# Kernel optimization log

Hardware: AMD Instinct MI355X
Metric: run time of the kernel (lower is better)

## Reference

```python
import jax, jax.numpy as jnp
import numpy as np

D_MODEL = 1024
B, T_Q, T_KV = 4, 2048, 2048


def _linear_params(key, d_in, d_out):
    kw, kb = jax.random.split(key)
    W = jax.random.normal(kw, (d_out, d_in), dtype=jnp.float32) * 0.02
    b = jax.random.normal(kb, (d_out,), dtype=jnp.float32) * 0.02
    return W, b


def setup_inputs() -> dict:
    key = jax.random.key(0)
    ks = jax.random.split(key, 7)
    latent_space = jax.random.normal(ks[0], (B, T_Q, D_MODEL), dtype=jnp.float32)
    input_space = jax.random.normal(ks[1], (B, T_KV, D_MODEL), dtype=jnp.float32)
    Wl, bl = _linear_params(ks[2], D_MODEL, D_MODEL)
    Wu, bu = _linear_params(ks[3], D_MODEL, D_MODEL)
    WA, bA = _linear_params(ks[4], D_MODEL, D_MODEL)  # A_proj: d -> J (J = d)
    WV, bV = _linear_params(ks[5], D_MODEL, D_MODEL)  # V_proj: J -> d
    Wo, bo = _linear_params(ks[6], D_MODEL, D_MODEL)
    return {
        "latent_space": latent_space, "input_space": input_space,
        "Wl": Wl, "bl": bl, "Wu": Wu, "bu": bu,
        "WA": WA, "bA": bA, "WV": WV, "bV": bV,
        "Wo": Wo, "bo": bo,
    }


def reference(latent_space, input_space, Wl, bl, Wu, bu, WA, bA, WV, bV, Wo, bo):
    # emb_0 = l_proj(latent)            [B, T_q, d]
    emb0 = jnp.einsum('bqd,ed->bqe', latent_space, Wl) + bl
    # l = softmax(u_proj(emb_0), -1)^T  [B, d, T_q]
    l = jax.nn.softmax(jnp.einsum('bqd,ed->bqe', emb0, Wu) + bu, axis=-1)
    l = jnp.swapaxes(l, -2, -1)
    # D = A_proj(input)                 [B, T_kv, J]
    Dm = jnp.einsum('bkd,jd->bkj', input_space, WA) + bA
    # A = softmax(V_proj(D), dim=-2)    softmax over T_kv
    A = jax.nn.softmax(jnp.einsum('bkj,dj->bkd', Dm, WV) + bV, axis=-2)
    # w = A @ l                         [B, T_kv, T_q]
    w = jnp.einsum('bkd,bdq->bkq', A, l)
    # o = w @ o_proj(latent)            [B, T_kv, d]
    ov = jnp.einsum('bqd,ed->bqe', latent_space, Wo) + bo
    o = jnp.einsum('bkq,bqd->bkd', w, ov)
    return o
```

## Files before the change

### kernel.cpp

```cpp
#include <hip/hip_runtime.h>
#include <hip/hip_bf16.h>
#include <stdint.h>

typedef __attribute__((ext_vector_type(8))) short bf16x8;
typedef __attribute__((ext_vector_type(4))) float f32x4;
typedef __attribute__((ext_vector_type(4))) unsigned short u16x4;

#define B_  4
#define T_  2048
#define D_  1024

__device__ __forceinline__ float bf2f(ushort u) {
  union { unsigned int i; float f; } v; v.i = ((unsigned int)u) << 16; return v.f;
}
__device__ __forceinline__ ushort f2bf(float f) {
  return (ushort)(__bfloat16_as_ushort(__float2bfloat16(f)));
}
__device__ __forceinline__ void async16(const void* g, void* l) {
  __builtin_amdgcn_global_load_lds(
      (const __attribute__((address_space(1))) void*)g,
      (__attribute__((address_space(3))) void*)l, 16, 0, 0);
}

__global__ __launch_bounds__(256)
void prep(const float* __restrict__ lat, const float* __restrict__ inp,
          const float* __restrict__ Wl, const float* __restrict__ bl,
          const float* __restrict__ Wu, const float* __restrict__ bu,
          const float* __restrict__ WA, const float* __restrict__ bA,
          const float* __restrict__ WV, const float* __restrict__ bV,
          const float* __restrict__ Wo, const float* __restrict__ bo,
          ushort* __restrict__ xBf, ushort* __restrict__ xBf2,
          ushort* __restrict__ w1, ushort* __restrict__ w2,
          ushort* __restrict__ wCatWo, float* __restrict__ bc, float* __restrict__ bc2,
          float* __restrict__ psum)
{
  __shared__ alignas(16) ushort t[64 * 65];
  const long NW = (long)D_ * D_;
  const int bx = blockIdx.x;
  const int tid = threadIdx.x;
  if (bx < 16384) {
    const float* in = bx < 8192 ? lat : inp;
    ushort* out = bx < 8192 ? xBf : xBf2;
    const long i = (long)(bx & 8191) * 256 + tid;
    const float4 v = *(const float4*)(in + i * 4);
    u16x4 o;
    o[0] = f2bf(v.x); o[1] = f2bf(v.y); o[2] = f2bf(v.z); o[3] = f2bf(v.w);
    *(u16x4*)(out + i * 4) = o;
  } else if (bx < 19456) {
    const int seg = (bx - 16384) >> 10;
    const float* in  = seg == 0 ? Wu : (seg == 1 ? WV : Wo);
    ushort* out = seg == 0 ? w1 : (seg == 1 ? w1 + NW : wCatWo);
    const long i = (long)((bx - 16384) & 1023) * 256 + tid;
    const float4 v = *(const float4*)(in + i * 4);
    u16x4 o;
    o[0] = f2bf(v.x); o[1] = f2bf(v.y); o[2] = f2bf(v.z); o[3] = f2bf(v.w);
    *(u16x4*)(out + i * 4) = o;
  } else if (bx < 19968) {
    const int z = (bx - 19456) >> 8;
    const int w = (bx - 19456) & 255;
    const float* in = z ? WA : Wl;
    ushort* out = z ? w2 + NW : w2;
    const int c0 = (w & 15) * 64, r0 = (w >> 4) * 64;
    const int tx = tid & 15, ty = tid >> 4;
#pragma unroll
    for (int i = 0; i < 4; ++i) {
      const int r = ty + i * 16;
      const float4 v = *(const float4*)(in + (long)(r0 + r) * D_ + c0 + tx * 4);
      t[(tx * 4 + 0) * 65 + r] = f2bf(v.x);
      t[(tx * 4 + 1) * 65 + r] = f2bf(v.y);
      t[(tx * 4 + 2) * 65 + r] = f2bf(v.z);
      t[(tx * 4 + 3) * 65 + r] = f2bf(v.w);
    }
    __syncthreads();
#pragma unroll
    for (int i = 0; i < 4; ++i) {
      const int c = ty + i * 16;
      u16x4 v;
#pragma unroll
      for (int j = 0; j < 4; ++j) v[j] = t[c * 65 + tx * 4 + j];
      *(u16x4*)(out + (long)(c0 + c) * D_ + r0 + tx * 4) = v;
    }
  } else if (bx < 20480) {
    const int z = (bx - 19968) >> 8;
    const int w = (bx - 19968) & 255;
    const float* W    = z ? WV : Wu;
    const float* bin  = z ? bA : bl;
    const float* badd = z ? bV : bu;
    float* out        = z ? bc2 : bc;
    const int wv = tid >> 6, lane = tid & 63;
    const int e = w * 4 + wv;
    const float* row = W + (long)e * D_;
    float s = 0.f;
#pragma unroll
    for (int i = 0; i < 16; ++i) s += row[lane + i * 64] * bin[lane + i * 64];
#pragma unroll
    for (int off = 32; off; off >>= 1) s += __shfl_xor(s, off);
    if (lane == 0) out[e] = s + badd[e];
  } else {
    psum[(bx - 20480) * 256 + tid] = 0.f;
  }
}

#define PH_SYNC_IN()                                               \
  __builtin_amdgcn_s_barrier();                                    \
  asm volatile("s_waitcnt lgkmcnt(0)" ::: "memory");               \
  __builtin_amdgcn_sched_barrier(0);                               \
  __builtin_amdgcn_s_setprio(1)
#define PH_SYNC_OUT()                                              \
  __builtin_amdgcn_s_setprio(0);                                   \
  __builtin_amdgcn_s_barrier()

__global__ __launch_bounds__(512, 2)
void gemm256(const ushort* __restrict__ A, const ushort* __restrict__ Bm,
             const float* __restrict__ bias1, const float* __restrict__ bias2,
             ushort* __restrict__ C1, ushort* __restrict__ C2,
             int ldA, int ldB)
{
  __shared__ alignas(16) ushort AbS[2 * 16384];
  __shared__ alignas(16) ushort BbS[3 * 16384];

  const int gx = gridDim.x;
  const int nwg = gx * gridDim.y;
  int fid = blockIdx.y * gx + blockIdx.x;
  fid = (fid & 7) * (nwg >> 3) + (fid >> 3);
  const int bx = fid % gx;
  const int by = fid / gx;
  const int tileM = by * 256, tileN = bx * 256;

  const int tid  = threadIdx.x;
  const int wid  = tid >> 6;
  const int lane = tid & 63;
  const int wm   = wid >> 2;
  const int wn   = wid & 3;

  const int srow8 = tid >> 3;
  const int scol8 = ((tid & 7) ^ (srow8 & 7)) << 3;
  const ushort* gAs = A  + (long)(tileM + srow8) * ldA + scol8;
  const ushort* gBs = Bm + (long)(tileN + srow8) * ldB + scol8;
  const int sdst = tid << 3;

#define STA(b, i, t) async16(gAs + (long)((i) * 64) * ldA + (t) * 64, \
                             AbS + (b) * 16384 + (i) * 4096 + sdst)
#define STB(b, i, t) async16(gBs + (long)((i) * 64) * ldB + (t) * 64, \
                             BbS + (b) * 16384 + (i) * 4096 + sdst)

  const int frow = lane & 15;
  const int kg   = lane >> 4;
  const int ck0 = ((kg       ^ (frow & 7)) << 3);
  const int ck1 = (((4 + kg) ^ (frow & 7)) << 3);
  int aoffr[8], boffr[4];
#pragma unroll
  for (int mi = 0; mi < 8; ++mi) aoffr[mi] = (wm * 128 + mi * 16 + frow) * 64;
#pragma unroll
  for (int n = 0; n < 4; ++n)    boffr[n]  = (wn * 64 + n * 16 + frow) * 64;

  f32x4 acc[8][4];
#pragma unroll
  for (int i = 0; i < 8; ++i)
#pragma unroll
    for (int j = 0; j < 4; ++j) acc[i][j] = (f32x4){0.f, 0.f, 0.f, 0.f};

#pragma unroll
  for (int i = 0; i < 4; ++i) STA(0, i, 0);
#pragma unroll
  for (int i = 0; i < 4; ++i) STB(0, i, 0);
#pragma unroll
  for (int i = 0; i < 4; ++i) STA(1, i, 1);
#pragma unroll
  for (int i = 0; i < 4; ++i) STB(1, i, 1);
  asm volatile("s_waitcnt vmcnt(8)" ::: "memory");
  __builtin_amdgcn_s_barrier();

#pragma unroll 1
  for (int t = 0; t < 16; ++t) {
    const int buf = t & 1;
    const int bB  = t - (t / 3) * 3;
    const int nA  = (t + 1) & 1;
    const int nB  = (t + 2) - ((t + 2) / 3) * 3;
    const ushort* Ac = AbS + buf * 16384;
    const ushort* Bc = BbS + bB * 16384;
    bf16x8 fa[4], fb[4], ga[4];

#pragma unroll
    for (int n = 0; n < 4; ++n) fb[n] = *(const bf16x8*)(Bc + boffr[n] + ck0);
#pragma unroll
    for (int m = 0; m < 4; ++m) fa[m] = *(const bf16x8*)(Ac + aoffr[m] + ck0);
    if (t >= 1 && t <= 14) { STA(nA, 0, t + 1); STA(nA, 1, t + 1); }
    PH_SYNC_IN();
#pragma unroll
    for (int m = 0; m < 4; ++m)
#pragma unroll
      for (int n = 0; n < 4; ++n)
        acc[m][n] = __builtin_amdgcn_mfma_f32_16x16x32_bf16(fa[m], fb[n], acc[m][n], 0, 0, 0);
    PH_SYNC_OUT();

#pragma unroll
    for (int m = 0; m < 4; ++m) ga[m] = *(const bf16x8*)(Ac + aoffr[4 + m] + ck0);
    if (t >= 1 && t <= 14) { STA(nA, 2, t + 1); STA(nA, 3, t + 1); }
    if (t <= 13)           { STB(nB, 0, t + 2); STB(nB, 1, t + 2); }
    PH_SYNC_IN();
#pragma unroll
    for (int m = 0; m < 4; ++m)
#pragma unroll
      for (int n = 0; n < 4; ++n)
        acc[4 + m][n] = __builtin_amdgcn_mfma_f32_16x16x32_bf16(ga[m], fb[n], acc[4 + m][n], 0, 0, 0);
    PH_SYNC_OUT();

#pragma unroll
    for (int n = 0; n < 4; ++n) fb[n] = *(const bf16x8*)(Bc + boffr[n] + ck1);
#pragma unroll
    for (int m = 0; m < 4; ++m) fa[m] = *(const bf16x8*)(Ac + aoffr[m] + ck1);
    if (t <= 13) { STB(nB, 2, t + 2); STB(nB, 3, t + 2); }
    PH_SYNC_IN();
#pragma unroll
    for (int m = 0; m < 4; ++m)
#pragma unroll
      for (int n = 0; n < 4; ++n)
        acc[m][n] = __builtin_amdgcn_mfma_f32_16x16x32_bf16(fa[m], fb[n], acc[m][n], 0, 0, 0);
    PH_SYNC_OUT();

#pragma unroll
    for (int m = 0; m < 4; ++m) ga[m] = *(const bf16x8*)(Ac + aoffr[4 + m] + ck1);
    if (t <= 13)      { asm volatile("s_waitcnt vmcnt(4)" ::: "memory"); }
    else if (t == 14) { asm volatile("s_waitcnt vmcnt(0)" ::: "memory"); }
    PH_SYNC_IN();
#pragma unroll
    for (int m = 0; m < 4; ++m)
#pragma unroll
      for (int n = 0; n < 4; ++n)
        acc[4 + m][n] = __builtin_amdgcn_mfma_f32_16x16x32_bf16(ga[m], fb[n], acc[4 + m][n], 0, 0, 0);
    PH_SYNC_OUT();
  }
#undef STA
#undef STB

  const bool second = tileN >= 1024;
  ushort* Cp = second ? C2 : C1;
  const float* bb = second ? bias2 : bias1;
  const int cb = tileN - (second ? 1024 : 0) + wn * 64 + (lane & 15);
  const int rb = tileM + wm * 128 + ((lane >> 4) << 2);
#pragma unroll
  for (int mi = 0; mi < 8; ++mi) {
    const int mrow = rb + mi * 16;
#pragma unroll
    for (int ni = 0; ni < 4; ++ni) {
      const int col = cb + ni * 16;
      const float bv = bb[col];
#pragma unroll
      for (int r = 0; r < 4; ++r)
        Cp[(long)(mrow + r) * 1024 + col] = f2bf(acc[mi][ni][r] + bv);
    }
  }
}

template<int MODE, int NKT = 16>
__global__ __launch_bounds__(512, 2)
void gemm128(const ushort* __restrict__ A, const ushort* __restrict__ Bm,
             const float* __restrict__ bias1, void* __restrict__ C1,
             int ldA, int ldB, long sAz, long sBz, long sCz,
             float* __restrict__ psumG)
{
  __shared__ alignas(16) ushort AbS[3 * 16384];
  __shared__ alignas(16) ushort BbS[3 * 8192];

  const int gx = gridDim.x, gy = gridDim.y;
  const int nwg = gx * gy * gridDim.z;
  int fid = (blockIdx.z * gy + blockIdx.y) * gx + blockIdx.x;
  fid = (fid & 7) * (nwg >> 3) + (fid >> 3);
  const int bx = fid % gx;
  const int by = (fid / gx) % gy;
  const int bz = fid / (gx * gy);
  const int tileM = by * 256, tileN = bx * 128;

  const ushort* Ap = A;
  const ushort* Bp = Bm;
  if constexpr (MODE == 2) {
    Ap += (long)(bz >> 1) * sAz + (long)(bz & 1) * 1024;
    Bp += (long)(bz >> 1) * sBz + (long)(bz & 1) * 1024;
  } else if constexpr (MODE == 4) {
    Ap += (long)(bz >> 2) * sAz + (long)(bz & 3) * 256;
    Bp += (long)(bz >> 2) * sBz + (long)(bz & 3) * 256;
  } else {
    Ap += (long)bz * sAz;
    Bp += (long)bz * sBz;
  }

  const int tid  = threadIdx.x;
  const int wid  = tid >> 6;
  const int lane = tid & 63;
  const int wm   = wid >> 1;
  const int wn   = wid & 1;

  const int srow8 = tid >> 3;
  const int scol8 = ((tid & 7) ^ (srow8 & 7)) << 3;
  const ushort* gAs = Ap + (long)(tileM + srow8) * ldA + scol8;
  const ushort* gBs = Bp + (long)(tileN + srow8) * ldB + scol8;
  const int sdst = tid << 3;

#define STA(b, i, t) async16(gAs + (long)((i) * 64) * ldA + (t) * 64, \
                             AbS + (b) * 16384 + (i) * 4096 + sdst)
#define STB(b, i, t) async16(gBs + (long)((i) * 64) * ldB + (t) * 64, \
                             BbS + (b) * 8192 + (i) * 4096 + sdst)

  const int frow = lane & 15;
  const int kg   = lane >> 4;
  const int ck0 = ((kg       ^ (frow & 7)) << 3);
  const int ck1 = (((4 + kg) ^ (frow & 7)) << 3);
  int aoffr[4], boffr[4];
#pragma unroll
  for (int mi = 0; mi < 4; ++mi) aoffr[mi] = (wm * 64 + mi * 16 + frow) * 64;
#pragma unroll
  for (int n = 0; n < 4; ++n)    boffr[n]  = (wn * 64 + n * 16 + frow) * 64;

  f32x4 acc[4][4];
#pragma unroll
  for (int i = 0; i < 4; ++i)
#pragma unroll
    for (int j = 0; j < 4; ++j) acc[i][j] = (f32x4){0.f, 0.f, 0.f, 0.f};

#pragma unroll
  for (int i = 0; i < 4; ++i) STA(0, i, 0);
  STB(0, 0, 0); STB(0, 1, 0);
#pragma unroll
  for (int i = 0; i < 4; ++i) STA(1, i, 1);
  STB(1, 0, 1); STB(1, 1, 1);
  asm volatile("s_waitcnt vmcnt(6)" ::: "memory");
  __builtin_amdgcn_s_barrier();

#pragma unroll 1
  for (int t = 0; t < NKT; ++t) {
    const int bufT = t - (t / 3) * 3;
    const int nb   = (t + 2) - ((t + 2) / 3) * 3;
    const ushort* Ac = AbS + bufT * 16384;
    const ushort* Bc = BbS + bufT * 8192;
    bf16x8 fa[4], fb[4];

#pragma unroll
    for (int n = 0; n < 4; ++n) fb[n] = *(const bf16x8*)(Bc + boffr[n] + ck0);
#pragma unroll
    for (int m = 0; m < 4; ++m) fa[m] = *(const bf16x8*)(Ac + aoffr[m] + ck0);
    if (t <= NKT - 3) { STA(nb, 0, t + 2); STA(nb, 1, t + 2); STA(nb, 2, t + 2); STA(nb, 3, t + 2); }
    PH_SYNC_IN();
#pragma unroll
    for (int m = 0; m < 4; ++m)
#pragma unroll
      for (int n = 0; n < 4; ++n)
        acc[m][n] = __builtin_amdgcn_mfma_f32_16x16x32_bf16(fa[m], fb[n], acc[m][n], 0, 0, 0);
    PH_SYNC_OUT();

#pragma unroll
    for (int n = 0; n < 4; ++n) fb[n] = *(const bf16x8*)(Bc + boffr[n] + ck1);
#pragma unroll
    for (int m = 0; m < 4; ++m) fa[m] = *(const bf16x8*)(Ac + aoffr[m] + ck1);
    if (t <= NKT - 3) { STB(nb, 0, t + 2); STB(nb, 1, t + 2); }
    if (t <= NKT - 3)      { asm volatile("s_waitcnt vmcnt(6)" ::: "memory"); }
    else if (t == NKT - 2) { asm volatile("s_waitcnt vmcnt(0)" ::: "memory"); }
    PH_SYNC_IN();
#pragma unroll
    for (int m = 0; m < 4; ++m)
#pragma unroll
      for (int n = 0; n < 4; ++n)
        acc[m][n] = __builtin_amdgcn_mfma_f32_16x16x32_bf16(fa[m], fb[n], acc[m][n], 0, 0, 0);
    PH_SYNC_OUT();
  }
#undef STA
#undef STB

  const int cb = tileN + wn * 64 + (lane & 15);
  const int rb = tileM + wm * 64 + ((lane >> 4) << 2);

  if constexpr (MODE == 1) {
    ushort* Cp = (ushort*)C1;
    const int bE = tileM >> 11;
#pragma unroll
    for (int ni = 0; ni < 4; ++ni) {
      const int col = cb + ni * 16;
      const float bv = bias1[col];
      float cs = 0.f;
#pragma unroll
      for (int mi = 0; mi < 4; ++mi)
#pragma unroll
        for (int r = 0; r < 4; ++r) {
          const ushort ev = f2bf(__expf(acc[mi][ni][r] + bv));
          Cp[(long)(rb + mi * 16 + r) * 1024 + col] = ev;
          cs += bf2f(ev);
        }
      cs += __shfl_xor(cs, 16);
      cs += __shfl_xor(cs, 32);
      if ((lane >> 4) == 0) atomicAdd(psumG + (long)bE * D_ + col, cs);
    }
  } else if constexpr (MODE == 2) {
    ushort* Cp = (ushort*)C1 + ((long)(bz & 1) * B_ + (bz >> 1)) * ((long)D_ * D_);
#pragma unroll
    for (int ni = 0; ni < 4; ++ni) {
      const int col = cb + ni * 16;
#pragma unroll
      for (int mi = 0; mi < 4; ++mi)
#pragma unroll
        for (int r = 0; r < 4; ++r)
          Cp[(long)(rb + mi * 16 + r) * 1024 + col] = f2bf(acc[mi][ni][r]);
    }
  } else if constexpr (MODE == 4) {
    const int comp = bz >> 2, sp = bz & 3;
    ushort* Cp = (ushort*)C1 + ((long)sp * 2 + comp) * ((long)D_ * D_);
#pragma unroll
    for (int ni = 0; ni < 4; ++ni) {
      const int col = cb + ni * 16;
#pragma unroll
      for (int mi = 0; mi < 4; ++mi)
#pragma unroll
        for (int r = 0; r < 4; ++r)
          Cp[(long)(rb + mi * 16 + r) * 1024 + col] = f2bf(acc[mi][ni][r]);
    }
  } else {
    float* Cp = (float*)C1 + (long)bz * sCz;
#pragma unroll
    for (int ni = 0; ni < 4; ++ni) {
      const int col = cb + ni * 16;
#pragma unroll
      for (int mi = 0; mi < 4; ++mi)
#pragma unroll
        for (int r = 0; r < 4; ++r)
          Cp[(long)(rb + mi * 16 + r) * 1024 + col] = acc[mi][ni][r];
    }
  }
}

__global__ __launch_bounds__(256)
void reduce4(const ushort* __restrict__ P, ushort* __restrict__ wCat)
{
  const long NW = (long)D_ * D_;
  const long i = ((long)blockIdx.x * 256 + threadIdx.x) * 8;
  float s[8] = {0.f, 0.f, 0.f, 0.f, 0.f, 0.f, 0.f, 0.f};
#pragma unroll
  for (int sp = 0; sp < 4; ++sp) {
    bf16x8 p = *(const bf16x8*)(P + (long)sp * 2 * NW + i);
#pragma unroll
    for (int j = 0; j < 8; ++j) s[j] += bf2f((ushort)p[j]);
  }
  const long comp = (i >= NW) ? 1 : 0;
  ushort* out = wCat + comp * 2 * NW + (i - comp * NW);
  bf16x8 o;
#pragma unroll
  for (int j = 0; j < 8; ++j) o[j] = (short)f2bf(s[j]);
  *(bf16x8*)out = o;
}

__global__ __launch_bounds__(256)
void rowexp_inv(const ushort* __restrict__ S, float* __restrict__ rinv)
{
  const long base = (long)blockIdx.x * D_;
  const int tid = threadIdx.x;
  float s = 0.f;
#pragma unroll
  for (int i = 0; i < 4; ++i) s += __expf(bf2f(S[base + i * 256 + tid]));
#pragma unroll
  for (int off = 32; off; off >>= 1) s += __shfl_xor(s, off);
  __shared__ float reds[4];
  if ((tid & 63) == 0) reds[tid >> 6] = s;
  __syncthreads();
  if (tid == 0) rinv[blockIdx.x] = 1.f / (reds[0] + reds[1] + reds[2] + reds[3]);
}

__global__ __launch_bounds__(256)
void transposeF(const ushort* __restrict__ l, ushort* __restrict__ lT,
                const ushort* __restrict__ ov, ushort* __restrict__ ovT,
                const float* __restrict__ rinv)
{
  __shared__ alignas(16) ushort t[64 * 65];
  const int z = blockIdx.z;
  const int b = z & (B_ - 1);
  const bool isL = z < B_;
  const ushort* in = (isL ? l : ov) + (long)b * T_ * D_;
  ushort* out      = (isL ? lT : ovT) + (long)b * (long)D_ * T_;
  const int c0 = blockIdx.x * 64, r0 = blockIdx.y * 64;
  const int tx = threadIdx.x & 15, ty = threadIdx.x >> 4;
#pragma unroll
  for (int i = 0; i < 4; ++i) {
    const int r = ty + i * 16;
    u16x4 v = *(const u16x4*)(in + (long)(r0 + r) * D_ + c0 + tx * 4);
    if (isL) {
      const float ri = rinv[(long)b * T_ + r0 + r];
#pragma unroll
      for (int c = 0; c < 4; ++c) t[(tx * 4 + c) * 65 + r] = f2bf(__expf(bf2f(v[c])) * ri);
    } else {
#pragma unroll
      for (int c = 0; c < 4; ++c) t[(tx * 4 + c) * 65 + r] = v[c];
    }
  }
  __syncthreads();
#pragma unroll
  for (int i = 0; i < 4; ++i) {
    const int c = ty + i * 16;
    u16x4 v;
#pragma unroll
    for (int j = 0; j < 4; ++j) v[j] = t[c * 65 + tx * 4 + j];
    *(u16x4*)(out + (long)(c0 + c) * T_ + r0 + tx * 4) = v;
  }
}

__global__ __launch_bounds__(256)
void reduce2_scale(const ushort* __restrict__ P, const float* __restrict__ psum,
                   ushort* __restrict__ MT)
{
  const long stride = (long)B_ * D_ * D_;
  const long base = ((long)blockIdx.x * 256 + threadIdx.x) * 8;
  const int b = (int)(base >> 20);
  const int e0 = (int)(base & (D_ - 1));
  bf16x8 p0 = *(const bf16x8*)(P + base);
  bf16x8 p1 = *(const bf16x8*)(P + stride + base);
  const float4 c0 = *(const float4*)(psum + (long)b * D_ + e0);
  const float4 c1 = *(const float4*)(psum + (long)b * D_ + e0 + 4);
  const float cc[8] = {1.f / c0.x, 1.f / c0.y, 1.f / c0.z, 1.f / c0.w,
                       1.f / c1.x, 1.f / c1.y, 1.f / c1.z, 1.f / c1.w};
  bf16x8 o;
#pragma unroll
  for (int j = 0; j < 8; ++j)
    o[j] = (short)f2bf((bf2f((ushort)p0[j]) + bf2f((ushort)p1[j])) * cc[j]);
  *(bf16x8*)(MT + base) = o;
}

extern "C" void kernel_launch(void* const* d_in, const int* in_sizes, int n_in,
                              void* d_out, int out_size, void* d_ws, size_t ws_size,
                              hipStream_t stream)
{
  (void)in_sizes; (void)n_in; (void)out_size; (void)ws_size;
  const float* lat = (const float*)d_in[0];
  const float* inp = (const float*)d_in[1];
  const float* Wl  = (const float*)d_in[2];
  const float* bl  = (const float*)d_in[3];
  const float* Wu  = (const float*)d_in[4];
  const float* bu  = (const float*)d_in[5];
  const float* WA  = (const float*)d_in[6];
  const float* bA  = (const float*)d_in[7];
  const float* WV  = (const float*)d_in[8];
  const float* bV  = (const float*)d_in[9];
  const float* Wo  = (const float*)d_in[10];
  const float* bo  = (const float*)d_in[11];

  char* w = (char*)d_ws;
  auto carve = [&](size_t bytes) { char* p = w; w += (bytes + 255) & ~(size_t)255; return p; };
  const long NT = (long)B_ * T_ * D_;
  const long NW = (long)D_ * D_;
  ushort* xBf   = (ushort*)carve(NT * 2);
  ushort* xBf2  = (ushort*)carve(NT * 2);
  ushort* bufA  = (ushort*)carve(NT * 2);
  ushort* bufB  = (ushort*)carve(NT * 2);
  ushort* scr   = (ushort*)carve(NT * 2);
  ushort* MT    = (ushort*)carve((long)B_ * NW * 2);
  ushort* wCat  = (ushort*)carve(3 * NW * 2);
  float*  bc    = (float*)carve(D_ * 4);
  float*  bc2   = (float*)carve(D_ * 4);
  float*  psum  = (float*)carve((long)B_ * D_ * 4);
  float*  rinv  = (float*)carve((long)B_ * T_ * 4);
  ushort* w1 = scr;
  ushort* w2 = scr + 2 * NW;
  ushort* Pc = bufA;
  ushort* ovT = scr;
  ushort* part = bufB;

  const dim3 blk(256, 1, 1);
  const dim3 blk5(512, 1, 1);

  prep<<<dim3(20496), blk, 0, stream>>>(lat, inp, Wl, bl, Wu, bu, WA, bA, WV, bV, Wo, bo,
                                        xBf, xBf2, w1, w2, wCat + NW, bc, bc2, psum);
  gemm128<4, 4><<<dim3(8, 4, 8), blk5, 0, stream>>>(
      w1, w2, nullptr, Pc, D_, D_, NW, NW, 0, nullptr);
  reduce4<<<dim3(1024), blk, 0, stream>>>(Pc, wCat);
  gemm256<<<dim3(8, 32, 1), blk5, 0, stream>>>(
      xBf, wCat, bc, bo, bufB, bufA, D_, D_);
  rowexp_inv<<<dim3(B_ * T_), blk, 0, stream>>>(bufB, rinv);
  transposeF<<<dim3(16, 32, 2 * B_), blk, 0, stream>>>(bufB, xBf, bufA, ovT, rinv);
  gemm128<2><<<dim3(8, 4, 8), blk5, 0, stream>>>(
      ovT, xBf, nullptr, part, T_, T_, (long)D_ * T_, (long)D_ * T_, 0, nullptr);
  gemm128<1><<<dim3(8, 32, 1), blk5, 0, stream>>>(
      xBf2, wCat + 2 * NW, bc2, bufA, D_, D_, 0, 0, 0, psum);
  reduce2_scale<<<dim3(2048), blk, 0, stream>>>(part, psum, MT);
  gemm128<3><<<dim3(8, 8, 4), blk5, 0, stream>>>(
      bufA, MT, nullptr, d_out, D_, D_,
      (long)T_ * D_, NW, (long)T_ * D_, nullptr);
}
```

Baseline: 292.0 us.

## Fuse row-exp sums into GEMM epilogue and merge two GEMMs into one launch

```diff
diff --git a/kernel.cpp b/kernel.cpp
--- a/kernel.cpp
+++ b/kernel.cpp
@@ -114,7 +114,7 @@
 void gemm256(const ushort* __restrict__ A, const ushort* __restrict__ Bm,
              const float* __restrict__ bias1, const float* __restrict__ bias2,
              ushort* __restrict__ C1, ushort* __restrict__ C2,
-             int ldA, int ldB)
+             int ldA, int ldB, float* __restrict__ rsumP)
 {
   __shared__ alignas(16) ushort AbS[2 * 16384];
   __shared__ alignas(16) ushort BbS[3 * 16384];
@@ -239,16 +239,46 @@
   const float* bb = second ? bias2 : bias1;
   const int cb = tileN - (second ? 1024 : 0) + wn * 64 + (lane & 15);
   const int rb = tileM + wm * 128 + ((lane >> 4) << 2);
-#pragma unroll
-  for (int mi = 0; mi < 8; ++mi) {
-    const int mrow = rb + mi * 16;
-#pragma unroll
-    for (int ni = 0; ni < 4; ++ni) {
-      const int col = cb + ni * 16;
-      const float bv = bb[col];
-#pragma unroll
-      for (int r = 0; r < 4; ++r)
-        Cp[(long)(mrow + r) * 1024 + col] = f2bf(acc[mi][ni][r] + bv);
+
+  if (!second) {
+    float bvv[4];
+#pragma unroll
+    for (int ni = 0; ni < 4; ++ni) bvv[ni] = bb[cb + ni * 16];
+    float* rsh = (float*)AbS;
+#pragma unroll
+    for (int mi = 0; mi < 8; ++mi) {
+      const int mrow = rb + mi * 16;
+#pragma unroll
+      for (int r = 0; r < 4; ++r) {
+        float s = 0.f;
+#pragma unroll
+        for (int ni = 0; ni < 4; ++ni) {
+          const ushort ev = f2bf(acc[mi][ni][r] + bvv[ni]);
+          Cp[(long)(mrow + r) * 1024 + cb + ni * 16] = ev;
+          s += __expf(bf2f(ev));
+        }
+        s += __shfl_xor(s, 1); s += __shfl_xor(s, 2);
+        s += __shfl_xor(s, 4); s += __shfl_xor(s, 8);
+        if ((lane & 15) == 0)
+          rsh[wn * 256 + (mrow + r - tileM)] = s;
+      }
+    }
+    __syncthreads();
+    if (tid < 256)
+      rsumP[(long)(tileN >> 8) * 8192 + tileM + tid] =
+          rsh[tid] + rsh[256 + tid] + rsh[512 + tid] + rsh[768 + tid];
+  } else {
+#pragma unroll
+    for (int mi = 0; mi < 8; ++mi) {
+      const int mrow = rb + mi * 16;
+#pragma unroll
+      for (int ni = 0; ni < 4; ++ni) {
+        const int col = cb + ni * 16;
+        const float bv = bb[col];
+#pragma unroll
+        for (int r = 0; r < 4; ++r)
+          Cp[(long)(mrow + r) * 1024 + col] = f2bf(acc[mi][ni][r] + bv);
+      }
     }
   }
 }
@@ -274,10 +304,7 @@
 
   const ushort* Ap = A;
   const ushort* Bp = Bm;
-  if constexpr (MODE == 2) {
-    Ap += (long)(bz >> 1) * sAz + (long)(bz & 1) * 1024;
-    Bp += (long)(bz >> 1) * sBz + (long)(bz & 1) * 1024;
-  } else if constexpr (MODE == 4) {
+  if constexpr (MODE == 4) {
     Ap += (long)(bz >> 2) * sAz + (long)(bz & 3) * 256;
     Bp += (long)(bz >> 2) * sBz + (long)(bz & 3) * 256;
   } else {
@@ -369,28 +396,168 @@
   const int cb = tileN + wn * 64 + (lane & 15);
   const int rb = tileM + wm * 64 + ((lane >> 4) << 2);
 
-  if constexpr (MODE == 1) {
-    ushort* Cp = (ushort*)C1;
-    const int bE = tileM >> 11;
+  if constexpr (MODE == 4) {
+    const int comp = bz >> 2, sp = bz & 3;
+    ushort* Cp = (ushort*)C1 + ((long)sp * 2 + comp) * ((long)D_ * D_);
 #pragma unroll
     for (int ni = 0; ni < 4; ++ni) {
       const int col = cb + ni * 16;
-      const float bv = bias1[col];
+#pragma unroll
+      for (int mi = 0; mi < 4; ++mi)
+#pragma unroll
+        for (int r = 0; r < 4; ++r)
+          Cp[(long)(rb + mi * 16 + r) * 1024 + col] = f2bf(acc[mi][ni][r]);
+    }
+  } else {
+    float* Cp = (float*)C1 + (long)bz * sCz;
+#pragma unroll
+    for (int ni = 0; ni < 4; ++ni) {
+      const int col = cb + ni * 16;
+#pragma unroll
+      for (int mi = 0; mi < 4; ++mi)
+#pragma unroll
+        for (int r = 0; r < 4; ++r)
+          Cp[(long)(rb + mi * 16 + r) * 1024 + col] = acc[mi][ni][r];
+    }
+  }
+}
+
+__global__ __launch_bounds__(512, 2)
+void gemm_me(const ushort* __restrict__ ovT, const ushort* __restrict__ lT,
+             ushort* __restrict__ part,
+             const ushort* __restrict__ xBf2, const ushort* __restrict__ wc2,
+             const float* __restrict__ bias2, ushort* __restrict__ Eout,
+             float* __restrict__ psumG)
+{
+  __shared__ alignas(16) ushort AbS[3 * 16384];
+  __shared__ alignas(16) ushort BbS[3 * 8192];
+
+  const int gx = gridDim.x, gy = gridDim.y;
+  const int nwg = gx * gy * gridDim.z;
+  int fid = (blockIdx.z * gy + blockIdx.y) * gx + blockIdx.x;
+  fid = (fid & 7) * (nwg >> 3) + (fid >> 3);
+  const int bx = fid % gx;
+  const int by = (fid / gx) % gy;
+  const int bz = fid / (gx * gy);
+
+  const bool isE = bz >= 8;
+  const int tileN = bx * 128;
+  int tileM;
+  const ushort* Ap; const ushort* Bp; long ld;
+  if (isE) {
+    tileM = ((bz - 8) * 4 + by) * 256;
+    Ap = xBf2; Bp = wc2; ld = 1024;
+  } else {
+    tileM = by * 256;
+    const long off = (long)(bz >> 1) * ((long)D_ * T_) + (long)(bz & 1) * 1024;
+    Ap = ovT + off; Bp = lT + off; ld = 2048;
+  }
+
+  const int tid  = threadIdx.x;
+  const int wid  = tid >> 6;
+  const int lane = tid & 63;
+  const int wm   = wid >> 1;
+  const int wn   = wid & 1;
+
+  const int srow8 = tid >> 3;
+  const int scol8 = ((tid & 7) ^ (srow8 & 7)) << 3;
+  const ushort* gAs = Ap + (long)(tileM + srow8) * ld + scol8;
+  const ushort* gBs = Bp + (long)(tileN + srow8) * ld + scol8;
+  const int sdst = tid << 3;
+
+#define STA(b, i, t) async16(gAs + (long)((i) * 64) * ld + (t) * 64, \
+                             AbS + (b) * 16384 + (i) * 4096 + sdst)
+#define STB(b, i, t) async16(gBs + (long)((i) * 64) * ld + (t) * 64, \
+                             BbS + (b) * 8192 + (i) * 4096 + sdst)
+
+  const int frow = lane & 15;
+  const int kg   = lane >> 4;
+  const int ck0 = ((kg       ^ (frow & 7)) << 3);
+  const int ck1 = (((4 + kg) ^ (frow & 7)) << 3);
+  int aoffr[4], boffr[4];
+#pragma unroll
+  for (int mi = 0; mi < 4; ++mi) aoffr[mi] = (wm * 64 + mi * 16 + frow) * 64;
+#pragma unroll
+  for (int n = 0; n < 4; ++n)    boffr[n]  = (wn * 64 + n * 16 + frow) * 64;
+
+  f32x4 acc[4][4];
+#pragma unroll
+  for (int i = 0; i < 4; ++i)
+#pragma unroll
+    for (int j = 0; j < 4; ++j) acc[i][j] = (f32x4){0.f, 0.f, 0.f, 0.f};
+
+#pragma unroll
+  for (int i = 0; i < 4; ++i) STA(0, i, 0);
+  STB(0, 0, 0); STB(0, 1, 0);
+#pragma unroll
+  for (int i = 0; i < 4; ++i) STA(1, i, 1);
+  STB(1, 0, 1); STB(1, 1, 1);
+  asm volatile("s_waitcnt vmcnt(6)" ::: "memory");
+  __builtin_amdgcn_s_barrier();
+
+#pragma unroll 1
+  for (int t = 0; t < 16; ++t) {
+    const int bufT = t - (t / 3) * 3;
+    const int nb   = (t + 2) - ((t + 2) / 3) * 3;
+    const ushort* Ac = AbS + bufT * 16384;
+    const ushort* Bc = BbS + bufT * 8192;
+    bf16x8 fa[4], fb[4];
+
+#pragma unroll
+    for (int n = 0; n < 4; ++n) fb[n] = *(const bf16x8*)(Bc + boffr[n] + ck0);
+#pragma unroll
+    for (int m = 0; m < 4; ++m) fa[m] = *(const bf16x8*)(Ac + aoffr[m] + ck0);
+    if (t <= 13) { STA(nb, 0, t + 2); STA(nb, 1, t + 2); STA(nb, 2, t + 2); STA(nb, 3, t + 2); }
+    PH_SYNC_IN();
+#pragma unroll
+    for (int m = 0; m < 4; ++m)
+#pragma unroll
+      for (int n = 0; n < 4; ++n)
+        acc[m][n] = __builtin_amdgcn_mfma_f32_16x16x32_bf16(fa[m], fb[n], acc[m][n], 0, 0, 0);
+    PH_SYNC_OUT();
+
+#pragma unroll
+    for (int n = 0; n < 4; ++n) fb[n] = *(const bf16x8*)(Bc + boffr[n] + ck1);
+#pragma unroll
+    for (int m = 0; m < 4; ++m) fa[m] = *(const bf16x8*)(Ac + aoffr[m] + ck1);
+    if (t <= 13) { STB(nb, 0, t + 2); STB(nb, 1, t + 2); }
+    if (t <= 13)      { asm volatile("s_waitcnt vmcnt(6)" ::: "memory"); }
+    else if (t == 14) { asm volatile("s_waitcnt vmcnt(0)" ::: "memory"); }
+    PH_SYNC_IN();
+#pragma unroll
+    for (int m = 0; m < 4; ++m)
+#pragma unroll
+      for (int n = 0; n < 4; ++n)
+        acc[m][n] = __builtin_amdgcn_mfma_f32_16x16x32_bf16(fa[m], fb[n], acc[m][n], 0, 0, 0);
+    PH_SYNC_OUT();
+  }
+#undef STA
+#undef STB
+
+  const int cb = tileN + wn * 64 + (lane & 15);
+  const int rb = tileM + wm * 64 + ((lane >> 4) << 2);
+
+  if (isE) {
+    const int bE = tileM >> 11;
+#pragma unroll
+    for (int ni = 0; ni < 4; ++ni) {
+      const int col = cb + ni * 16;
+      const float bv = bias2[col];
       float cs = 0.f;
 #pragma unroll
       for (int mi = 0; mi < 4; ++mi)
 #pragma unroll
         for (int r = 0; r < 4; ++r) {
           const ushort ev = f2bf(__expf(acc[mi][ni][r] + bv));
-          Cp[(long)(rb + mi * 16 + r) * 1024 + col] = ev;
+          Eout[(long)(rb + mi * 16 + r) * 1024 + col] = ev;
           cs += bf2f(ev);
         }
       cs += __shfl_xor(cs, 16);
       cs += __shfl_xor(cs, 32);
       if ((lane >> 4) == 0) atomicAdd(psumG + (long)bE * D_ + col, cs);
     }
-  } else if constexpr (MODE == 2) {
-    ushort* Cp = (ushort*)C1 + ((long)(bz & 1) * B_ + (bz >> 1)) * ((long)D_ * D_);
+  } else {
+    ushort* Cp = part + ((long)(bz & 1) * B_ + (bz >> 1)) * ((long)D_ * D_);
 #pragma unroll
     for (int ni = 0; ni < 4; ++ni) {
       const int col = cb + ni * 16;
@@ -399,29 +566,6 @@
 #pragma unroll
         for (int r = 0; r < 4; ++r)
           Cp[(long)(rb + mi * 16 + r) * 1024 + col] = f2bf(acc[mi][ni][r]);
-    }
-  } else if constexpr (MODE == 4) {
-    const int comp = bz >> 2, sp = bz & 3;
-    ushort* Cp = (ushort*)C1 + ((long)sp * 2 + comp) * ((long)D_ * D_);
-#pragma unroll
-    for (int ni = 0; ni < 4; ++ni) {
-      const int col = cb + ni * 16;
-#pragma unroll
-      for (int mi = 0; mi < 4; ++mi)
-#pragma unroll
-        for (int r = 0; r < 4; ++r)
-          Cp[(long)(rb + mi * 16 + r) * 1024 + col] = f2bf(acc[mi][ni][r]);
-    }
-  } else {
-    float* Cp = (float*)C1 + (long)bz * sCz;
-#pragma unroll
-    for (int ni = 0; ni < 4; ++ni) {
-      const int col = cb + ni * 16;
-#pragma unroll
-      for (int mi = 0; mi < 4; ++mi)
-#pragma unroll
-        for (int r = 0; r < 4; ++r)
-          Cp[(long)(rb + mi * 16 + r) * 1024 + col] = acc[mi][ni][r];
     }
   }
 }
@@ -447,25 +591,9 @@
 }
 
 __global__ __launch_bounds__(256)
-void rowexp_inv(const ushort* __restrict__ S, float* __restrict__ rinv)
-{
-  const long base = (long)blockIdx.x * D_;
-  const int tid = threadIdx.x;
-  float s = 0.f;
-#pragma unroll
-  for (int i = 0; i < 4; ++i) s += __expf(bf2f(S[base + i * 256 + tid]));
-#pragma unroll
-  for (int off = 32; off; off >>= 1) s += __shfl_xor(s, off);
-  __shared__ float reds[4];
-  if ((tid & 63) == 0) reds[tid >> 6] = s;
-  __syncthreads();
-  if (tid == 0) rinv[blockIdx.x] = 1.f / (reds[0] + reds[1] + reds[2] + reds[3]);
-}
-
-__global__ __launch_bounds__(256)
 void transposeF(const ushort* __restrict__ l, ushort* __restrict__ lT,
                 const ushort* __restrict__ ov, ushort* __restrict__ ovT,
-                const float* __restrict__ rinv)
+                const float* __restrict__ rsumP)
 {
   __shared__ alignas(16) ushort t[64 * 65];
   const int z = blockIdx.z;
@@ -480,7 +608,9 @@
     const int r = ty + i * 16;
     u16x4 v = *(const u16x4*)(in + (long)(r0 + r) * D_ + c0 + tx * 4);
     if (isL) {
-      const float ri = rinv[(long)b * T_ + r0 + r];
+      const long gr = (long)b * T_ + r0 + r;
+      const float ri = 1.f / (rsumP[gr] + rsumP[8192 + gr] +
+                              rsumP[16384 + gr] + rsumP[24576 + gr]);
 #pragma unroll
       for (int c = 0; c < 4; ++c) t[(tx * 4 + c) * 65 + r] = f2bf(__expf(bf2f(v[c])) * ri);
     } else {
@@ -552,7 +682,7 @@
   float*  bc    = (float*)carve(D_ * 4);
   float*  bc2   = (float*)carve(D_ * 4);
   float*  psum  = (float*)carve((long)B_ * D_ * 4);
-  float*  rinv  = (float*)carve((long)B_ * T_ * 4);
+  float*  rsumP = (float*)carve(4L * B_ * T_ * 4);
   ushort* w1 = scr;
   ushort* w2 = scr + 2 * NW;
   ushort* Pc = bufA;
@@ -568,13 +698,10 @@
       w1, w2, nullptr, Pc, D_, D_, NW, NW, 0, nullptr);
   reduce4<<<dim3(1024), blk, 0, stream>>>(Pc, wCat);
   gemm256<<<dim3(8, 32, 1), blk5, 0, stream>>>(
-      xBf, wCat, bc, bo, bufB, bufA, D_, D_);
-  rowexp_inv<<<dim3(B_ * T_), blk, 0, stream>>>(bufB, rinv);
-  transposeF<<<dim3(16, 32, 2 * B_), blk, 0, stream>>>(bufB, xBf, bufA, ovT, rinv);
-  gemm128<2><<<dim3(8, 4, 8), blk5, 0, stream>>>(
-      ovT, xBf, nullptr, part, T_, T_, (long)D_ * T_, (long)D_ * T_, 0, nullptr);
-  gemm128<1><<<dim3(8, 32, 1), blk5, 0, stream>>>(
-      xBf2, wCat + 2 * NW, bc2, bufA, D_, D_, 0, 0, 0, psum);
+      xBf, wCat, bc, bo, bufB, bufA, D_, D_, rsumP);
+  transposeF<<<dim3(16, 32, 2 * B_), blk, 0, stream>>>(bufB, xBf, bufA, ovT, rsumP);
+  gemm_me<<<dim3(8, 4, 16), blk5, 0, stream>>>(
+      ovT, xBf, part, xBf2, wCat + 2 * NW, bc2, bufA, psum);
   reduce2_scale<<<dim3(2048), blk, 0, stream>>>(part, psum, MT);
   gemm128<3><<<dim3(8, 8, 4), blk5, 0, stream>>>(
       bufA, MT, nullptr, d_out, D_, D_,
```

After: 288.0 us. Within noise of the previous version (-1.4%).
